# Performance work log

Measured on AMD Instinct MI355X. Metric: run time of the kernel, lower is better.

## Reference

```python
import jax, jax.numpy as jnp
import numpy as np


def setup_inputs() -> dict:
    key = jax.random.key(0)
    k1, k2 = jax.random.split(key)
    B, N, C, K = 8, 8192, 64, 16
    x = jax.random.normal(k1, (B, N, C), dtype=jnp.float32)
    idx = jax.random.randint(k2, (B, N, K), 0, N, dtype=jnp.int64)
    return {"x": x, "idx": idx}


def reference(x, idx):
    # x: (B, N, C) points; idx: (B, N, k) per-batch neighbor indices in [0, N)
    B, N, C = x.shape
    k = idx.shape[2]
    # gather neighbor features: (B, N, k, C)
    feature = jax.vmap(lambda xb, ib: xb[ib])(x, idx)
    # center point broadcast to (B, N, k, C)
    center = jnp.broadcast_to(x[:, :, None, :], (B, N, k, C))
    # edge features: concat(neighbor - center, center) along channel -> (B, N, k, 2C)
    out = jnp.concatenate([feature - center, center], axis=3)
    # permute to (B, N, 2C, k)
    return out.transpose(0, 1, 3, 2)
```

## Files before the change

kernel.cpp:

```cpp
#include <hip/hip_runtime.h>


constexpr int N = 8192;
constexpr int C = 64;
constexpr int K = 16;
constexpr int PAD = 68;

__global__ __launch_bounds__(256) void edge_feature_kernel(
    const float* __restrict__ x,
    const int*   __restrict__ idx,
    float*       __restrict__ out) {
  const int point = blockIdx.x;
  const int b     = point >> 13;
  const int tid   = threadIdx.x;

  __shared__ float s_nb[K * PAD];
  __shared__ float s_c[C];
  __shared__ int   s_idx[K];

  if (tid < K) s_idx[tid] = idx[(size_t)point * K + tid];
  if (tid >= 64 && tid < 64 + C) s_c[tid - 64] = x[(size_t)point * C + (tid - 64)];
  __syncthreads();

  {
    const int k  = tid >> 4;
    const int c4 = tid & 15;
    const size_t row_base = ((size_t)b * N + (size_t)s_idx[k]) * C;
    float4 v = reinterpret_cast<const float4*>(x + row_base)[c4];
    *reinterpret_cast<float4*>(s_nb + k * PAD + c4 * 4) = v;
  }
  __syncthreads();

  float4* op4 = reinterpret_cast<float4*>(out + (size_t)point * (2 * C * K));
  #pragma unroll
  for (int i = 0; i < 2; ++i) {
    const int f     = tid + i * 256;
    const int c2    = f >> 2;
    const int kbase = (f & 3) * 4;
    float4 v;
    if (c2 < C) {
      const float cen = s_c[c2];
      v.x = s_nb[(kbase + 0) * PAD + c2] - cen;
      v.y = s_nb[(kbase + 1) * PAD + c2] - cen;
      v.z = s_nb[(kbase + 2) * PAD + c2] - cen;
      v.w = s_nb[(kbase + 3) * PAD + c2] - cen;
    } else {
      const float cen = s_c[c2 - C];
      v = make_float4(cen, cen, cen, cen);
    }
    op4[f] = v;
  }
}

extern "C" void kernel_launch(void* const* d_in, const int* in_sizes, int n_in,
                              void* d_out, int out_size, void* d_ws, size_t ws_size,
                              hipStream_t stream) {
  const float* x   = (const float*)d_in[0];
  const int*   idx = (const int*)d_in[1];
  float*       out = (float*)d_out;

  const int B = 8;
  const int n_points = B * N;
  edge_feature_kernel<<<n_points, 256, 0, stream>>>(x, idx, out);
}
```

Baseline: 562.0 us.

## Process four points per block with swizzled block order and nontemporal stores

Each block now handles four points instead of one. Each thread issues its four index loads and four neighbor-row gathers before writing them to shared memory, which raises memory-level parallelism and removes one barrier. Block IDs are remapped across eight groups so that concurrently running blocks cover different batch regions, which is likely meant to spread blocks across XCDs and their L2 caches. Output is written with nontemporal stores so the 256MB write stream does not pollute the cache. Center values are now read straight from global memory rather than staged through shared memory.

```diff
diff --git a/kernel.cpp b/kernel.cpp
--- a/kernel.cpp
+++ b/kernel.cpp
@@ -1,54 +1,71 @@
 #include <hip/hip_runtime.h>
 
 
-constexpr int N = 8192;
-constexpr int C = 64;
-constexpr int K = 16;
-constexpr int PAD = 68;
+typedef float f32x4 __attribute__((ext_vector_type(4)));
+
+constexpr int NPTS = 8192;
+constexpr int C    = 64;
+constexpr int K    = 16;
+constexpr int P    = 4;
+constexpr int PAD  = 68;
+constexpr int NB   = 8;
 
 __global__ __launch_bounds__(256) void edge_feature_kernel(
     const float* __restrict__ x,
     const int*   __restrict__ idx,
     float*       __restrict__ out) {
-  const int point = blockIdx.x;
-  const int b     = point >> 13;
-  const int tid   = threadIdx.x;
+  const int nwg = (NB * NPTS) / P;
+  const int cpx = nwg >> 3;
+  const int bid = blockIdx.x;
+  const int swz = (bid & 7) * cpx + (bid >> 3);
+  const int point0 = swz * P;
+  const int b   = point0 >> 13;
+  const int tid = threadIdx.x;
 
-  __shared__ float s_nb[K * PAD];
-  __shared__ float s_c[C];
-  __shared__ int   s_idx[K];
+  __shared__ float s_nb[P * K * PAD];
 
-  if (tid < K) s_idx[tid] = idx[(size_t)point * K + tid];
-  if (tid >= 64 && tid < 64 + C) s_c[tid - 64] = x[(size_t)point * C + (tid - 64)];
+  const int k  = tid >> 4;
+  const int c4 = tid & 15;
+
+  int nk[P];
+  #pragma unroll
+  for (int i = 0; i < P; ++i)
+    nk[i] = idx[(size_t)(point0 + i) * K + k];
+
+  f32x4 v[P];
+  #pragma unroll
+  for (int i = 0; i < P; ++i) {
+    const size_t rb = ((size_t)b * NPTS + (size_t)nk[i]) * C;
+    v[i] = reinterpret_cast<const f32x4*>(x + rb)[c4];
+  }
+
+  #pragma unroll
+  for (int i = 0; i < P; ++i)
+    *reinterpret_cast<f32x4*>(s_nb + (i * K + k) * PAD + c4 * 4) = v[i];
+
   __syncthreads();
 
-  {
-    const int k  = tid >> 4;
-    const int c4 = tid & 15;
-    const size_t row_base = ((size_t)b * N + (size_t)s_idx[k]) * C;
-    float4 v = reinterpret_cast<const float4*>(x + row_base)[c4];
-    *reinterpret_cast<float4*>(s_nb + k * PAD + c4 * 4) = v;
-  }
-  __syncthreads();
-
-  float4* op4 = reinterpret_cast<float4*>(out + (size_t)point * (2 * C * K));
+  f32x4* op4 = reinterpret_cast<f32x4*>(out) + (size_t)point0 * (2 * C * K / 4);
   #pragma unroll
-  for (int i = 0; i < 2; ++i) {
-    const int f     = tid + i * 256;
-    const int c2    = f >> 2;
-    const int kbase = (f & 3) * 4;
-    float4 v;
+  for (int i = 0; i < 2 * P; ++i) {
+    const int f  = i * 256 + tid;
+    const int p  = f >> 9;
+    const int fi = f & 511;
+    const int c2 = fi >> 2;
+    const int kb = (fi & 3) * 4;
+    f32x4 w;
     if (c2 < C) {
-      const float cen = s_c[c2];
-      v.x = s_nb[(kbase + 0) * PAD + c2] - cen;
-      v.y = s_nb[(kbase + 1) * PAD + c2] - cen;
-      v.z = s_nb[(kbase + 2) * PAD + c2] - cen;
-      v.w = s_nb[(kbase + 3) * PAD + c2] - cen;
+      const float cen = x[(size_t)(point0 + p) * C + c2];
+      const float* sp = s_nb + (p * K + kb) * PAD + c2;
+      w.x = sp[0 * PAD] - cen;
+      w.y = sp[1 * PAD] - cen;
+      w.z = sp[2 * PAD] - cen;
+      w.w = sp[3 * PAD] - cen;
     } else {
-      const float cen = s_c[c2 - C];
-      v = make_float4(cen, cen, cen, cen);
+      const float cen = x[(size_t)(point0 + p) * C + (c2 - C)];
+      w = (f32x4){cen, cen, cen, cen};
     }
-    op4[f] = v;
+    __builtin_nontemporal_store(w, op4 + f);
   }
 }
 
@@ -59,7 +76,6 @@
   const int*   idx = (const int*)d_in[1];
   float*       out = (float*)d_out;
 
-  const int B = 8;
-  const int n_points = B * N;
-  edge_feature_kernel<<<n_points, 256, 0, stream>>>(x, idx, out);
+  const int n_blocks = (NB * NPTS) / P;
+  edge_feature_kernel<<<n_blocks, 256, 0, stream>>>(x, idx, out);
 }
```

Measured after the change: 539.7 us. 4.0% less time.
